# Optimization experiments

Measured on AMD Instinct MI355X. Metric: run time of the kernel, lower is better.

Reference implementation:

```python
import jax, jax.numpy as jnp
import numpy as np

B, N, F_, CI, C, CO = 2, 1024, 2048, 3, 80, 128
NB = 15          # DirResNet blocks
Q = C // 4


def _graph_bn(x, g, b, eps=1e-5):
    # BatchNorm over channels with stats over (batch, nodes) -- training-mode batch stats
    mu = jnp.mean(x, axis=(0, 1), keepdims=True)
    var = jnp.var(x, axis=(0, 1), keepdims=True)
    return (x - mu) * jax.lax.rsqrt(var + eps) * g + b


def _graph_conv(L, x, W0, W1, bias):
    # GraphConv with k=1: linear on [x, L @ x]
    return x @ W0 + jnp.einsum('bnm,bmc->bnc', L, x) @ W1 + bias


def _forward(inputs, L, Di, DiA, mask,
             conv1_W0, conv1_W1, conv1_b,
             rn_bn0_g, rn_bn0_b, rn_fc0_W, rn_fc0_b,
             rn_bn1_g, rn_bn1_b, rn_fc1_W, rn_fc1_b,
             bn1_g, bn1_b, bn2_g, bn2_b, bn3_g, bn3_b,
             conv2_W0, conv2_W1, conv2_b):
    v = _graph_conv(L, inputs, conv1_W0, conv1_W1, conv1_b)      # [B,N,C]
    f = jnp.zeros((B, F_, C), v.dtype)
    z = jnp.zeros_like(v)
    carry = (f, f, v, z, z)  # [f, tmp_f, v, tmp_v, tmp_v]

    def block(carry, p):
        f, tmp_f, v, tv0, tv1 = carry
        g0, b0, W0, c0, g1, b1, W1, c1 = p
        # Dirac: vertices -> faces (quaternion reshape: [B,N,C] -> [B,4N,C/4])
        Dv = jnp.matmul(Di, v.reshape(B, 4 * N, Q)).reshape(B, F_, C)
        x = jnp.concatenate([f, Dv], axis=-1)                    # [B,F,2C]
        f_new = jax.nn.elu(_graph_bn(x, g0, b0) @ W0 + c0) + tmp_f
        # Adjoint Dirac: faces -> vertices
        Df = jnp.matmul(DiA, f_new.reshape(B, 4 * F_, Q)).reshape(B, N, C)
        y = jnp.concatenate([v, Df], axis=-1)                    # [B,N,2C]
        v_new = jax.nn.elu(_graph_bn(y, g1, b1) @ W1 + c1) + tv0
        return (f_new, f, v_new, v, tv0), None

    carry, _ = jax.lax.scan(
        block, carry,
        (rn_bn0_g, rn_bn0_b, rn_fc0_W, rn_fc0_b,
         rn_bn1_g, rn_bn1_b, rn_fc1_W, rn_fc1_b))
    _, _, v2, v1, v0 = carry
    v = jax.nn.elu(_graph_bn(v2, bn1_g, bn1_b)
                   + _graph_bn(v1, bn2_g, bn2_b)
                   + _graph_bn(v0, bn3_g, bn3_b))
    # Dropout2d: identity (eval mode / deterministic reference)
    v = _graph_conv(L, v, conv2_W0, conv2_W1, conv2_b)           # [B,N,CO]
    out = (v * mask).sum(axis=1) / mask.sum(axis=1)              # masked mean pool -> [B,CO]
    return out


def setup_inputs() -> dict:
    key = jax.random.key(0)
    ks = jax.random.split(key, 32)
    s = 0.05
    d = {
        'inputs': jax.random.normal(ks[0], (B, N, CI), jnp.float32),
        'L': jax.random.normal(ks[1], (B, N, N), jnp.float32) / np.float32(np.sqrt(N)),
        'Di': jax.random.normal(ks[2], (B, 4 * F_, 4 * N), jnp.float32) / np.float32(np.sqrt(4 * N)),
        'DiA': jax.random.normal(ks[3], (B, 4 * N, 4 * F_), jnp.float32) / np.float32(np.sqrt(4 * F_)),
        'mask': (jax.random.uniform(ks[4], (B, N, 1)) > 0.2).astype(jnp.float32),
        'conv1_W0': jax.random.normal(ks[5], (CI, C), jnp.float32) * s,
        'conv1_W1': jax.random.normal(ks[6], (CI, C), jnp.float32) * s,
        'conv1_b': jax.random.normal(ks[7], (C,), jnp.float32) * s,
        'rn_bn0_g': 1.0 + 0.1 * jax.random.normal(ks[8], (NB, 2 * C), jnp.float32),
        'rn_bn0_b': s * jax.random.normal(ks[9], (NB, 2 * C), jnp.float32),
        'rn_fc0_W': jax.random.normal(ks[10], (NB, 2 * C, C), jnp.float32) * s,
        'rn_fc0_b': jax.random.normal(ks[11], (NB, C), jnp.float32) * s,
        'rn_bn1_g': 1.0 + 0.1 * jax.random.normal(ks[12], (NB, 2 * C), jnp.float32),
        'rn_bn1_b': s * jax.random.normal(ks[13], (NB, 2 * C), jnp.float32),
        'rn_fc1_W': jax.random.normal(ks[14], (NB, 2 * C, C), jnp.float32) * s,
        'rn_fc1_b': jax.random.normal(ks[15], (NB, C), jnp.float32) * s,
        'bn1_g': 1.0 + 0.1 * jax.random.normal(ks[16], (C,), jnp.float32),
        'bn1_b': s * jax.random.normal(ks[17], (C,), jnp.float32),
        'bn2_g': 1.0 + 0.1 * jax.random.normal(ks[18], (C,), jnp.float32),
        'bn2_b': s * jax.random.normal(ks[19], (C,), jnp.float32),
        'bn3_g': 1.0 + 0.1 * jax.random.normal(ks[20], (C,), jnp.float32),
        'bn3_b': s * jax.random.normal(ks[21], (C,), jnp.float32),
        'conv2_W0': jax.random.normal(ks[22], (C, CO), jnp.float32) * s,
        'conv2_W1': jax.random.normal(ks[23], (C, CO), jnp.float32) * s,
        'conv2_b': jax.random.normal(ks[24], (CO,), jnp.float32) * s,
    }
    return d


def reference(inputs, L, Di, DiA, mask,
              conv1_W0, conv1_W1, conv1_b,
              rn_bn0_g, rn_bn0_b, rn_fc0_W, rn_fc0_b,
              rn_bn1_g, rn_bn1_b, rn_fc1_W, rn_fc1_b,
              bn1_g, bn1_b, bn2_g, bn2_b, bn3_g, bn3_b,
              conv2_W0, conv2_W1, conv2_b):
    return _forward(inputs, L, Di, DiA, mask,
                    conv1_W0, conv1_W1, conv1_b,
                    rn_bn0_g, rn_bn0_b, rn_fc0_W, rn_fc0_b,
                    rn_bn1_g, rn_bn1_b, rn_fc1_W, rn_fc1_b,
                    bn1_g, bn1_b, bn2_g, bn2_b, bn3_g, bn3_b,
                    conv2_W0, conv2_W1, conv2_b)
```

## Files before the change

### kernel.cpp

```cpp
#include <hip/hip_runtime.h>
#include <cstdint>

#define BB 2
#define NN 1024
#define FF 2048
#define CC 80
#define C2 160
#define NB_ 15
#define ROWS_X (BB*FF)
#define ROWS_Y (BB*NN)
#define WTP 168

typedef __attribute__((ext_vector_type(8))) _Float16 half8;
typedef __attribute__((ext_vector_type(4))) _Float16 half4;
typedef __attribute__((ext_vector_type(4))) float f32x4;

__device__ __forceinline__ void softbar() {
  __builtin_amdgcn_sched_barrier(0);
  asm volatile("s_waitcnt lgkmcnt(0)" ::: "memory");
  __builtin_amdgcn_s_barrier();
  __builtin_amdgcn_sched_barrier(0);
}

__global__ __launch_bounds__(256) void k_conv1(
    const float* __restrict__ inp, const float* __restrict__ L,
    const float* __restrict__ W0, const float* __restrict__ W1,
    const float* __restrict__ bias, float* __restrict__ v,
    float4* __restrict__ vstat)
{
  int bx = blockIdx.x;
  int b = bx >> 6, rb = bx & 63;
  int row0 = rb * 16;
  __shared__ float red[256][3];
  __shared__ float lx[16][3];
  __shared__ float st[16][2][CC];
  int t = threadIdx.x;
  int rloc = t >> 4, sl = t & 15;
  const float* Lrow = L + ((size_t)b*NN + row0 + rloc) * NN;
  const float* ipb  = inp + (size_t)b*NN*3;
  float a0=0.f,a1=0.f,a2=0.f;
  for (int m = sl; m < NN; m += 16) {
    float lv = Lrow[m];
    a0 = fmaf(lv, ipb[m*3+0], a0);
    a1 = fmaf(lv, ipb[m*3+1], a1);
    a2 = fmaf(lv, ipb[m*3+2], a2);
  }
  red[t][0]=a0; red[t][1]=a1; red[t][2]=a2;
  __syncthreads();
  if (t < 48) {
    int row = t/3, ci = t%3;
    float s=0.f;
    for (int s2=0; s2<16; ++s2) s += red[row*16+s2][ci];
    lx[row][ci]=s;
  }
  __syncthreads();
  for (int o = t; o < 16*CC; o += 256) {
    int row = o/CC, c = o%CC;
    const float* ir = inp + ((size_t)b*NN + row0 + row)*3;
    float val = bias[c];
    #pragma unroll
    for (int ci=0; ci<3; ++ci)
      val += ir[ci]*W0[ci*CC+c] + lx[row][ci]*W1[ci*CC+c];
    v[((size_t)b*NN + row0 + row)*CC + c] = val;
    st[row][0][c] = val;
    st[row][1][c] = val*val;
  }
  __syncthreads();
  if (t < 40) {
    float s0=0.f,q0=0.f,s1=0.f,q1=0.f;
    for (int row=0; row<16; ++row){
      s0+=st[row][0][2*t];   q0+=st[row][1][2*t];
      s1+=st[row][0][2*t+1]; q1+=st[row][1][2*t+1];
    }
    vstat[(size_t)bx*40 + t] = make_float4(s0,q0,s1,q1);
  }
}

template<bool CVT>
__global__ __launch_bounds__(256) __attribute__((amdgpu_waves_per_eu(2,2)))
void k_dirac_mfma(
    const void* __restrict__ Ain, _Float16* __restrict__ Aout,
    const float* __restrict__ x,
    float* __restrict__ y, float4* __restrict__ stat, int M, int K)
{
  int b = blockIdx.y;
  x += (size_t)b*(size_t)K*20; y += (size_t)b*(size_t)M*20;
  const _Float16* Ah = (const _Float16*)Ain + (size_t)b*M*K;
  const float*    Af = (const float*)Ain    + (size_t)b*M*K;
  _Float16* Ao = CVT ? (Aout + (size_t)b*M*K) : nullptr;
  __shared__ _Float16 xT[2][2][32][264];
  __shared__ float cb_[2][8][64];
  __shared__ float stS[2][CC], stQ[2][CC];
  int t = threadIdx.x, lane = t & 63, w = t >> 6;
  int rw = w & 1, kh = w >> 1;
  int row0 = blockIdx.x*32 + rw*16;
  int cl = lane & 15, cg = lane >> 4;
  int KH = K >> 1;
  f32x4 acc0 = {0.f,0.f,0.f,0.f}, acc1 = {0.f,0.f,0.f,0.f};
  const float4* xv = (const float4*)x;
  int nchunk = KH >> 8;
  size_t aoff = (size_t)(row0 + cl)*K + (size_t)kh*KH + cg*8;

  for (int i = t; i < 2*2*12*264; i += 256) {
    int bb = i / (2*12*264);
    int rem = i - bb*(2*12*264);
    int hh = rem / (12*264);
    int r2 = rem - hh*(12*264);
    xT[bb][hh][20 + r2/264][r2 % 264] = (_Float16)0.f;
  }
  {
    float4 s0[5], s1[5];
    #pragma unroll
    for (int i=0;i<5;++i){ s0[i]=xv[(size_t)t*5+i]; s1[i]=xv[((size_t)KH+t)*5+i]; }
    #pragma unroll
    for (int i=0;i<5;++i){
      xT[0][0][4*i+0][t]=(_Float16)s0[i].x; xT[0][0][4*i+1][t]=(_Float16)s0[i].y;
      xT[0][0][4*i+2][t]=(_Float16)s0[i].z; xT[0][0][4*i+3][t]=(_Float16)s0[i].w;
      xT[0][1][4*i+0][t]=(_Float16)s1[i].x; xT[0][1][4*i+1][t]=(_Float16)s1[i].y;
      xT[0][1][4*i+2][t]=(_Float16)s1[i].z; xT[0][1][4*i+3][t]=(_Float16)s1[i].w;
    }
  }
  half8 a_cur[8];
  if constexpr (!CVT) {
    #pragma unroll
    for (int ks=0;ks<8;++ks) a_cur[ks] = *(const half8*)(Ah + aoff + ks*32);
  }
  __syncthreads();

  for (int c=0; c<nchunk; ++c) {
    int cur = c & 1;
    bool more = (c+1 < nchunk);
    float4 s0[5], s1[5];
    half8 a_nxt[8];
    if (more) {
      size_t k0 = (size_t)(c+1)*256 + t;
      #pragma unroll
      for (int i=0;i<5;++i){ s0[i]=xv[k0*5+i]; s1[i]=xv[(k0+KH)*5+i]; }
      if constexpr (!CVT) {
        const _Float16* An = Ah + aoff + (size_t)(c+1)*256;
        #pragma unroll
        for (int ks=0;ks<8;++ks) a_nxt[ks] = *(const half8*)(An + ks*32);
      }
    }
    if constexpr (CVT) {
      size_t ao = aoff + (size_t)c*256;
      #pragma unroll
      for (int ks=0;ks<8;++ks) {
        float4 f0 = *(const float4*)(Af + ao + ks*32);
        float4 f1 = *(const float4*)(Af + ao + ks*32 + 4);
        half8 a;
        a[0]=(_Float16)f0.x; a[1]=(_Float16)f0.y; a[2]=(_Float16)f0.z; a[3]=(_Float16)f0.w;
        a[4]=(_Float16)f1.x; a[5]=(_Float16)f1.y; a[6]=(_Float16)f1.z; a[7]=(_Float16)f1.w;
        a_cur[ks] = a;
        *(half8*)(Ao + ao + ks*32) = a;
      }
    }
    #pragma unroll
    for (int ks=0;ks<8;++ks) {
      half8 b0 = *(const half8*)(&xT[cur][kh][cl     ][ks*32 + cg*8]);
      half8 b1 = *(const half8*)(&xT[cur][kh][16 + cl][ks*32 + cg*8]);
      acc0 = __builtin_amdgcn_mfma_f32_16x16x32_f16(a_cur[ks], b0, acc0, 0,0,0);
      acc1 = __builtin_amdgcn_mfma_f32_16x16x32_f16(a_cur[ks], b1, acc1, 0,0,0);
    }
    if (more) {
      #pragma unroll
      for (int i=0;i<5;++i){
        xT[cur^1][0][4*i+0][t]=(_Float16)s0[i].x; xT[cur^1][0][4*i+1][t]=(_Float16)s0[i].y;
        xT[cur^1][0][4*i+2][t]=(_Float16)s0[i].z; xT[cur^1][0][4*i+3][t]=(_Float16)s0[i].w;
        xT[cur^1][1][4*i+0][t]=(_Float16)s1[i].x; xT[cur^1][1][4*i+1][t]=(_Float16)s1[i].y;
        xT[cur^1][1][4*i+2][t]=(_Float16)s1[i].z; xT[cur^1][1][4*i+3][t]=(_Float16)s1[i].w;
      }
      if constexpr (!CVT) {
        #pragma unroll
        for (int ks=0;ks<8;++ks) a_cur[ks] = a_nxt[ks];
      }
    }
    softbar();
  }

  if (kh == 1) {
    #pragma unroll
    for (int j=0;j<4;++j){ cb_[rw][j][lane]=acc0[j]; cb_[rw][4+j][lane]=acc1[j]; }
  }
  __syncthreads();
  if (kh == 0) {
    #pragma unroll
    for (int j=0;j<4;++j){ acc0[j]+=cb_[rw][j][lane]; acc1[j]+=cb_[rw][4+j][lane]; }
    #pragma unroll
    for (int j=0;j<4;++j) {
      float v = acc0[j];
      y[(size_t)(row0 + 4*cg + j)*20 + cl] = v;
      float s = v, sq = v*v;
      s  += __shfl_xor(s,16);  s  += __shfl_xor(s,32);
      sq += __shfl_xor(sq,16); sq += __shfl_xor(sq,32);
      if (cg==0) { stS[rw][j*20+cl]=s; stQ[rw][j*20+cl]=sq; }
    }
    #pragma unroll
    for (int j=0;j<4;++j) {
      float v = acc1[j];
      if (cl < 4) y[(size_t)(row0 + 4*cg + j)*20 + 16 + cl] = v;
      float s = v, sq = v*v;
      s  += __shfl_xor(s,16);  s  += __shfl_xor(s,32);
      sq += __shfl_xor(sq,16); sq += __shfl_xor(sq,32);
      if (cg==0 && cl<4) { stS[rw][j*20+16+cl]=s; stQ[rw][j*20+16+cl]=sq; }
    }
  }
  __syncthreads();
  int slot = blockIdx.y*gridDim.x + blockIdx.x;
  if (t < 40) {
    float4 o;
    o.x = stS[0][2*t]  +stS[1][2*t];
    o.y = stQ[0][2*t]  +stQ[1][2*t];
    o.z = stS[0][2*t+1]+stS[1][2*t+1];
    o.w = stQ[0][2*t+1]+stQ[1][2*t+1];
    stat[(size_t)slot*40 + t] = o;
  }
}

__global__ __launch_bounds__(256) __attribute__((amdgpu_waves_per_eu(2,2)))
void k_dirac_f32(
    const float* __restrict__ A, const float* __restrict__ x,
    float* __restrict__ y, float4* __restrict__ stat, int M, int K)
{
  const int DR = 4;
  int b = blockIdx.y;
  A += (size_t)b*M*K; x += (size_t)b*(size_t)K*20; y += (size_t)b*(size_t)M*20;
  __shared__ float xs[2][20][256];
  __shared__ float stS[4][CC], stQ[4][CC];
  int t = threadIdx.x, lane = t & 63, w = t >> 6;
  int row0 = blockIdx.x*(4*DR) + w*DR;
  float acc[DR][20];
  #pragma unroll
  for (int r=0;r<DR;++r)
    #pragma unroll
    for (int q=0;q<20;++q) acc[r][q]=0.f;
  const float4* xv = (const float4*)x;
  int nchunk = K >> 8;
  const float* Abase = A + (size_t)row0*K + (lane<<2);
  {
    float4 s0[5];
    #pragma unroll
    for (int i=0;i<5;++i) s0[i] = xv[(size_t)t*5 + i];
    #pragma unroll
    for (int i=0;i<5;++i) {
      xs[0][4*i+0][t]=s0[i].x; xs[0][4*i+1][t]=s0[i].y;
      xs[0][4*i+2][t]=s0[i].z; xs[0][4*i+3][t]=s0[i].w;
    }
  }
  float4 a[DR];
  #pragma unroll
  for (int r=0;r<DR;++r) a[r] = *(const float4*)(Abase + (size_t)r*K);
  __syncthreads();
  for (int c=0; c<nchunk; ++c) {
    int cur = c & 1;
    bool more = (c+1 < nchunk);
    float4 st[5];
    if (more) {
      size_t kb = (size_t)(c+1)*256 + t;
      #pragma unroll
      for (int i=0;i<5;++i) st[i] = xv[kb*5 + i];
    }
    float4 af[DR];
    #pragma unroll
    for (int r=0;r<DR;++r) af[r] = a[r];
    if (more) {
      const float* An = Abase + (size_t)(c+1)*256;
      #pragma unroll
      for (int r=0;r<DR;++r) a[r] = *(const float4*)(An + (size_t)r*K);
    }
    #pragma unroll
    for (int q=0;q<20;++q) {
      float4 xq = *(const float4*)(&xs[cur][q][lane<<2]);
      #pragma unroll
      for (int r=0;r<DR;++r) {
        acc[r][q] = fmaf(af[r].x, xq.x, acc[r][q]);
        acc[r][q] = fmaf(af[r].y, xq.y, acc[r][q]);
        acc[r][q] = fmaf(af[r].z, xq.z, acc[r][q]);
        acc[r][q] = fmaf(af[r].w, xq.w, acc[r][q]);
      }
    }
    if (more) {
      #pragma unroll
      for (int i=0;i<5;++i) {
        xs[cur^1][4*i+0][t]=st[i].x; xs[cur^1][4*i+1][t]=st[i].y;
        xs[cur^1][4*i+2][t]=st[i].z; xs[cur^1][4*i+3][t]=st[i].w;
      }
    }
    __syncthreads();
  }
  #pragma unroll
  for (int r=0;r<DR;++r) {
    #pragma unroll
    for (int q=0;q<20;++q) {
      float s = acc[r][q];
      s += __shfl_xor(s, 1);  s += __shfl_xor(s, 2);
      s += __shfl_xor(s, 4);  s += __shfl_xor(s, 8);
      s += __shfl_xor(s, 16); s += __shfl_xor(s, 32);
      acc[r][q]=s;
    }
    if (lane==0) {
      float4* yp = (float4*)(y + (size_t)(row0+r)*20);
      yp[0] = make_float4(acc[r][0],acc[r][1],acc[r][2],acc[r][3]);
      yp[1] = make_float4(acc[r][4],acc[r][5],acc[r][6],acc[r][7]);
      yp[2] = make_float4(acc[r][8],acc[r][9],acc[r][10],acc[r][11]);
      yp[3] = make_float4(acc[r][12],acc[r][13],acc[r][14],acc[r][15]);
      yp[4] = make_float4(acc[r][16],acc[r][17],acc[r][18],acc[r][19]);
    }
  }
  if (lane == 0) {
    #pragma unroll
    for (int r=0;r<DR;++r)
      #pragma unroll
      for (int q=0;q<20;++q) {
        float v0 = acc[r][q];
        stS[w][r*20+q] = v0;
        stQ[w][r*20+q] = v0*v0;
      }
  }
  __syncthreads();
  int slot = blockIdx.y*gridDim.x + blockIdx.x;
  if (t < 40) {
    float4 o;
    o.x = stS[0][2*t]+stS[1][2*t]+stS[2][2*t]+stS[3][2*t];
    o.y = stQ[0][2*t]+stQ[1][2*t]+stQ[2][2*t]+stQ[3][2*t];
    o.z = stS[0][2*t+1]+stS[1][2*t+1]+stS[2][2*t+1]+stS[3][2*t+1];
    o.w = stQ[0][2*t+1]+stQ[1][2*t+1]+stQ[2][2*t+1]+stQ[3][2*t+1];
    stat[(size_t)slot*40 + t] = o;
  }
}

__global__ __launch_bounds__(320) void k_fc(
    const float* __restrict__ p1, const float* __restrict__ p2,
    const float4* __restrict__ sp1, int ns1,
    const float4* __restrict__ sp2, int ns2,
    const float* __restrict__ g, const float* __restrict__ bb,
    const float* __restrict__ W, const float* __restrict__ cb,
    const float* add, float* out,
    float4* __restrict__ statout, int rows, float invrows)
{
  __shared__ _Float16 Wt[80*WTP];
  __shared__ _Float16 xh[16*WTP];
  __shared__ float ad[2][C2];
  __shared__ float bpl[CC];
  __shared__ float4 pst[2][2][40];
  __shared__ float stS[CC], stQ[CC];
  int t = threadIdx.x;
  int lane = t & 63, wv = t >> 6;
  int cl = lane & 15, cg = lane >> 4;
  int r0 = blockIdx.x * 16;

  if (t < 160) {
    int p = t % 40, s = (t/40) & 1, h = t/80;
    const float4* sp = s ? sp2 : sp1;
    int ns = s ? ns2 : ns1;
    int half = ns >> 1;
    const float4* base = sp + (size_t)(h*half)*40 + p;
    float4 acc = {0.f,0.f,0.f,0.f};
    int i=0;
    for (; i+8<=half; i+=8) {
      float4 v[8];
      #pragma unroll
      for (int j=0;j<8;++j) v[j] = base[(size_t)(i+j)*40];
      #pragma unroll
      for (int j=0;j<8;++j){ acc.x+=v[j].x; acc.y+=v[j].y; acc.z+=v[j].z; acc.w+=v[j].w; }
    }
    for (; i<half; ++i){
      float4 v = base[(size_t)i*40];
      acc.x+=v.x; acc.y+=v.y; acc.z+=v.z; acc.w+=v.w;
    }
    pst[h][s][p] = acc;
  } else {
    int t2 = t - 160;
    #pragma unroll
    for (int i=0;i<20;++i) {
      int f4 = t2 + i*160;
      float4 w4 = ((const float4*)W)[f4];
      int c2 = f4/20, c = (f4%20)*4;
      Wt[(c+0)*WTP + c2] = (_Float16)w4.x;
      Wt[(c+1)*WTP + c2] = (_Float16)w4.y;
      Wt[(c+2)*WTP + c2] = (_Float16)w4.z;
      Wt[(c+3)*WTP + c2] = (_Float16)w4.w;
    }
  }
  __syncthreads();

  half8 bfr[5];
  #pragma unroll
  for (int ks=0;ks<5;++ks)
    bfr[ks] = *(const half8*)(&Wt[(wv*16+cl)*WTP + ks*32 + cg*8]);
  if (t < C2) {
    int s = (t < CC) ? 0 : 1;
    int chl = (t < CC) ? t : t - CC;
    int p = chl >> 1, e = chl & 1;
    float4 a0 = pst[0][s][p], a1 = pst[1][s][p];
    float S = e ? (a0.z + a1.z) : (a0.x + a1.x);
    float Q = e ? (a0.w + a1.w) : (a0.y + a1.y);
    float mean = S*invrows;
    float var  = fmaf(-mean, mean, Q*invrows);
    float aa   = g[t]*rsqrtf(var + 1e-5f);
    ad[0][t]=aa; ad[1][t]= bb[t] - mean*aa;
  }
  __syncthreads();

  #pragma unroll
  for (int i=0;i<2;++i) {
    int f4 = t + i*320;
    if (f4 < 640) {
      int row = f4/40, cq = (f4%40)*4;
      const float* src = (cq < 80) ? (p1 + (size_t)(r0+row)*CC + cq)
                                   : (p2 + (size_t)(r0+row)*CC + cq - 80);
      float4 x4 = *(const float4*)src;
      half4 h4;
      h4[0]=(_Float16)(x4.x*ad[0][cq+0]); h4[1]=(_Float16)(x4.y*ad[0][cq+1]);
      h4[2]=(_Float16)(x4.z*ad[0][cq+2]); h4[3]=(_Float16)(x4.w*ad[0][cq+3]);
      *(half4*)(&xh[row*WTP + cq]) = h4;
    }
  }
  if (t < CC) {
    float s = cb[t];
    #pragma unroll
    for (int ks=0;ks<20;++ks) {
      half8 w8 = *(const half8*)(&Wt[t*WTP + ks*8]);
      #pragma unroll
      for (int j=0;j<8;++j) s = fmaf(ad[1][ks*8+j], (float)w8[j], s);
    }
    bpl[t]=s;
  }
  __syncthreads();

  half8 afr[5];
  #pragma unroll
  for (int ks=0;ks<5;++ks)
    afr[ks] = *(const half8*)(&xh[cl*WTP + ks*32 + cg*8]);
  f32x4 acc = {0.f,0.f,0.f,0.f};
  #pragma unroll
  for (int ks=0;ks<5;++ks)
    acc = __builtin_amdgcn_mfma_f32_16x16x32_f16(afr[ks], bfr[ks], acc, 0,0,0);
  float ss=0.f, sq=0.f;
  int col = wv*16 + cl;
  #pragma unroll
  for (int j=0;j<4;++j) {
    int row = r0 + 4*cg + j;
    float val = acc[j] + bpl[col];
    val = val>0.f ? val : expm1f(val);
    val += add[(size_t)row*CC + col];
    out[(size_t)row*CC + col] = val;
    ss += val; sq = fmaf(val,val,sq);
  }
  ss += __shfl_xor(ss,16); ss += __shfl_xor(ss,32);
  sq += __shfl_xor(sq,16); sq += __shfl_xor(sq,32);
  if (cg==0) { stS[col]=ss; stQ[col]=sq; }
  __syncthreads();
  if (t < 40)
    statout[(size_t)blockIdx.x*40 + t] = make_float4(stS[2*t], stQ[2*t], stS[2*t+1], stQ[2*t+1]);
}

__global__ __launch_bounds__(256) void k_final(
    const float* __restrict__ v2, const float* __restrict__ v1, const float* __restrict__ v0,
    const float4* __restrict__ s2, const float4* __restrict__ s1, const float4* __restrict__ s0,
    const float* __restrict__ g1, const float* __restrict__ b1,
    const float* __restrict__ g2, const float* __restrict__ b2,
    const float* __restrict__ g3, const float* __restrict__ b3,
    float* __restrict__ vf, int ns)
{
  __shared__ float A[3][CC], D[3][CC];
  __shared__ float4 pf[2][3][40];
  int t = threadIdx.x;
  if (t < 240) {
    int p = t % 40, s = (t/40) % 3, h = t/120;
    const float4* sp = s==0 ? s2 : (s==1 ? s1 : s0);
    int half = ns >> 1;
    const float4* base = sp + (size_t)(h*half)*40 + p;
    float4 acc = {0.f,0.f,0.f,0.f};
    int i=0;
    for (; i+8<=half; i+=8) {
      float4 v[8];
      #pragma unroll
      for (int j=0;j<8;++j) v[j] = base[(size_t)(i+j)*40];
      #pragma unroll
      for (int j=0;j<8;++j){ acc.x+=v[j].x; acc.y+=v[j].y; acc.z+=v[j].z; acc.w+=v[j].w; }
    }
    for (; i<half; ++i){
      float4 v = base[(size_t)i*40];
      acc.x+=v.x; acc.y+=v.y; acc.z+=v.z; acc.w+=v.w;
    }
    pf[h][s][p] = acc;
  }
  __syncthreads();
  if (t < 240) {
    int set = t/80, chl = t%80, p = chl>>1, e = chl&1;
    const float* gg  = set==0? g1 : (set==1? g2 : g3);
    const float* bbp = set==0? b1 : (set==1? b2 : b3);
    float4 a0 = pf[0][set][p], a1 = pf[1][set][p];
    float S = e ? (a0.z + a1.z) : (a0.x + a1.x);
    float Q = e ? (a0.w + a1.w) : (a0.y + a1.y);
    float mean = S*(1.f/ROWS_Y);
    float var  = fmaf(-mean,mean,Q*(1.f/ROWS_Y));
    float aa   = gg[chl]*rsqrtf(var+1e-5f);
    A[set][chl]=aa; D[set][chl]=bbp[chl]-mean*aa;
  }
  __syncthreads();
  for (size_t idx = (size_t)blockIdx.x*256 + t; idx < (size_t)ROWS_Y*CC; idx += (size_t)gridDim.x*256) {
    int c = (int)(idx % CC);
    float val = fmaf(v2[idx],A[0][c],D[0][c]) + fmaf(v1[idx],A[1][c],D[1][c]) + fmaf(v0[idx],A[2][c],D[2][c]);
    vf[idx] = val>0.f? val : expm1f(val);
  }
}

__global__ __launch_bounds__(256) void k_w(
    const float* __restrict__ mask, const float* __restrict__ L, float* __restrict__ w)
{
  int bx = blockIdx.x;
  int b = bx >> 4, n0 = (bx & 15) * 64;
  int t = threadIdx.x;
  int ks = t >> 6;
  __shared__ float red[4][64];
  float acc=0.f;
  const float* Lb = L + (size_t)b*NN*NN;
  const float* mb = mask + b*NN;
  int n = n0 + (t & 63);
  for (int k = ks*256; k < ks*256+256; k+=8) {
    float mv[8], lv[8];
    #pragma unroll
    for (int j=0;j<8;++j){ mv[j]=mb[k+j]; lv[j]=Lb[(size_t)(k+j)*NN + n]; }
    #pragma unroll
    for (int j=0;j<8;++j) acc = fmaf(mv[j], lv[j], acc);
  }
  red[ks][t&63]=acc;
  __syncthreads();
  if (t < 64) w[b*NN + n0 + t] = red[0][t]+red[1][t]+red[2][t]+red[3][t];
}

__global__ __launch_bounds__(256) void k_pool(
    const float* __restrict__ vf, const float* __restrict__ mask,
    const float* __restrict__ w, float* __restrict__ part)
{
  int bx = blockIdx.x;
  int b = bx >> 3, slab = bx & 7;
  int t = threadIdx.x, c = t%CC, rs = t/CC;
  __shared__ float st[3][2][CC];
  if (t<240) {
    float a1=0.f,a2=0.f;
    for (int r = rs; r < 128; r += 3) {
      int row = slab*128 + r;
      float val = vf[((size_t)b*NN + row)*CC + c];
      a1 = fmaf(mask[b*NN+row], val, a1);
      a2 = fmaf(w[b*NN+row],    val, a2);
    }
    st[rs][0][c]=a1; st[rs][1][c]=a2;
  }
  __syncthreads();
  if (t<CC) {
    part[((b*8+slab)*2+0)*CC+t] = st[0][0][t]+st[1][0][t]+st[2][0][t];
    part[((b*8+slab)*2+1)*CC+t] = st[0][1][t]+st[1][1][t]+st[2][1][t];
  }
}

__global__ __launch_bounds__(256) void k_out(
    const float* __restrict__ part, const float* __restrict__ mask,
    const float* __restrict__ W0, const float* __restrict__ W1,
    const float* __restrict__ b2, float* __restrict__ outp)
{
  __shared__ float pl[2][2][CC];
  __shared__ float msred[2][128];
  __shared__ float ms[2];
  int t = threadIdx.x;
  {
    int b = t >> 7, k0 = t & 127;
    float m[8];
    #pragma unroll
    for (int j=0;j<8;++j) m[j] = mask[b*NN + k0 + j*128];
    msred[b][k0] = ((m[0]+m[1])+(m[2]+m[3]))+((m[4]+m[5])+(m[6]+m[7]));
  }
  if (t < 160) {
    int b = t/CC, c = t%CC;
    float v1[8], v2[8];
    #pragma unroll
    for (int slab=0; slab<8; ++slab){
      v1[slab] = part[((b*8+slab)*2+0)*CC+c];
      v2[slab] = part[((b*8+slab)*2+1)*CC+c];
    }
    float s1=0.f,s2=0.f;
    #pragma unroll
    for (int slab=0;slab<8;++slab){ s1+=v1[slab]; s2+=v2[slab]; }
    pl[b][0][c]=s1; pl[b][1][c]=s2;
  }
  __syncthreads();
  if (t < 2) {
    float s=0.f;
    for (int k=0;k<128;++k) s += msred[t][k];
    ms[t]=s;
  }
  __syncthreads();
  int b = t >> 7, co = t & 127;
  float acc = 0.f;
  for (int c=0;c<CC;c+=8) {
    float w0[8], w1[8];
    #pragma unroll
    for (int j=0;j<8;++j){ w0[j]=W0[(c+j)*128+co]; w1[j]=W1[(c+j)*128+co]; }
    #pragma unroll
    for (int j=0;j<8;++j) acc += pl[b][0][c+j]*w0[j] + pl[b][1][c+j]*w1[j];
  }
  outp[t] = acc/ms[b] + b2[co];
}

extern "C" void kernel_launch(void* const* d_in, const int* in_sizes, int n_in,
                              void* d_out, int out_size, void* d_ws, size_t ws_size,
                              hipStream_t stream)
{
  const float* inp  = (const float*)d_in[0];
  const float* L    = (const float*)d_in[1];
  const float* Di   = (const float*)d_in[2];
  const float* DiA  = (const float*)d_in[3];
  const float* mask = (const float*)d_in[4];
  const float* c1W0 = (const float*)d_in[5];
  const float* c1W1 = (const float*)d_in[6];
  const float* c1b  = (const float*)d_in[7];
  const float* bn0g = (const float*)d_in[8];
  const float* bn0b = (const float*)d_in[9];
  const float* fc0W = (const float*)d_in[10];
  const float* fc0b = (const float*)d_in[11];
  const float* bn1g = (const float*)d_in[12];
  const float* bn1b = (const float*)d_in[13];
  const float* fc1W = (const float*)d_in[14];
  const float* fc1b = (const float*)d_in[15];
  const float* fbn1g= (const float*)d_in[16];
  const float* fbn1b= (const float*)d_in[17];
  const float* fbn2g= (const float*)d_in[18];
  const float* fbn2b= (const float*)d_in[19];
  const float* fbn3g= (const float*)d_in[20];
  const float* fbn3b= (const float*)d_in[21];
  const float* c2W0 = (const float*)d_in[22];
  const float* c2W1 = (const float*)d_in[23];
  const float* c2b  = (const float*)d_in[24];

  float* ws = (float*)d_ws;
  size_t off = 0;
  auto alloc = [&](size_t n)->float* { float* p = ws + off; off += (n + 63) & ~(size_t)63; return p; };
  const size_t STFL = (size_t)1024*40*4;
  float* vb[3];   for (int i=0;i<3;++i) vb[i]   = alloc((size_t)BB*NN*CC);
  float* fb[2];   for (int i=0;i<2;++i) fb[i]   = alloc((size_t)BB*FF*CC);
  float* Dv       = alloc((size_t)BB*FF*CC);
  float* Df       = alloc((size_t)BB*NN*CC);
  float4* vstat[3];for (int i=0;i<3;++i) vstat[i]= (float4*)alloc(STFL);
  float4* fstat[2];for (int i=0;i<2;++i) fstat[i]= (float4*)alloc(STFL);
  float4* dvstat  = (float4*)alloc(STFL);
  float4* dfstat  = (float4*)alloc(STFL);
  float* vf       = alloc((size_t)BB*NN*CC);
  float* wv       = alloc((size_t)BB*NN);
  float* part     = alloc((size_t)16*2*CC);
  const size_t nDi = (size_t)BB*(4*FF)*(4*NN);
  _Float16* Dih  = (_Float16*)alloc(nDi/2);
  _Float16* DiAh = (_Float16*)alloc(nDi/2);
  bool usebf = (off*sizeof(float) <= ws_size);

  hipMemsetAsync(fb[0],    0, (size_t)BB*FF*CC*4, stream);
  hipMemsetAsync(fb[1],    0, (size_t)BB*FF*CC*4, stream);
  hipMemsetAsync(vb[1],    0, (size_t)BB*NN*CC*4, stream);
  hipMemsetAsync(fstat[0], 0, (size_t)256*40*16, stream);

  k_conv1<<<128,256,0,stream>>>(inp, L, c1W0, c1W1, c1b, vb[0], vstat[0]);

  int nsDv = usebf ? 512 : 1024;
  int nsDf = usebf ? 256 : 512;
  int cur=0, p1=1, p2=2, fcur=0, fs=0;
  for (int it=0; it<NB_; ++it) {
    if (usebf) {
      if (it==0) k_dirac_mfma<true ><<<dim3(256,2),256,0,stream>>>(Di,  Dih, vb[cur], Dv, dvstat, 4*FF, 4*NN);
      else       k_dirac_mfma<false><<<dim3(256,2),256,0,stream>>>(Dih, Dih, vb[cur], Dv, dvstat, 4*FF, 4*NN);
    } else {
      k_dirac_f32<<<dim3(512,2),256,0,stream>>>(Di, vb[cur], Dv, dvstat, 4*FF, 4*NN);
    }
    k_fc<<<ROWS_X/16,320,0,stream>>>(fb[fcur], Dv, fstat[fs],256, dvstat,nsDv,
        bn0g+(size_t)it*C2, bn0b+(size_t)it*C2, fc0W+(size_t)it*C2*CC, fc0b+(size_t)it*CC,
        fb[1-fcur], fb[1-fcur], fstat[1-fs], ROWS_X, 1.f/ROWS_X);
    fcur = 1-fcur; fs = 1-fs;
    if (usebf) {
      if (it==0) k_dirac_mfma<true ><<<dim3(128,2),256,0,stream>>>(DiA,  DiAh, fb[fcur], Df, dfstat, 4*NN, 4*FF);
      else       k_dirac_mfma<false><<<dim3(128,2),256,0,stream>>>(DiAh, DiAh, fb[fcur], Df, dfstat, 4*NN, 4*FF);
    } else {
      k_dirac_f32<<<dim3(256,2),256,0,stream>>>(DiA, fb[fcur], Df, dfstat, 4*NN, 4*FF);
    }
    k_fc<<<ROWS_Y/16,320,0,stream>>>(vb[cur], Df, vstat[cur],128, dfstat,nsDf,
        bn1g+(size_t)it*C2, bn1b+(size_t)it*C2, fc1W+(size_t)it*C2*CC, fc1b+(size_t)it*CC,
        vb[p1], vb[p2], vstat[p2], ROWS_Y, 1.f/ROWS_Y);
    int tmp=p2; p2=p1; p1=cur; cur=tmp;
  }

  k_final<<<128,256,0,stream>>>(vb[cur],vb[p1],vb[p2], vstat[cur],vstat[p1],vstat[p2],
      fbn1g,fbn1b,fbn2g,fbn2b,fbn3g,fbn3b, vf, 128);
  k_w<<<32,256,0,stream>>>(mask, L, wv);
  k_pool<<<16,256,0,stream>>>(vf, mask, wv, part);
  k_out<<<1,256,0,stream>>>(part, mask, c2W0, c2W1, c2b, (float*)d_out);
}
```

Before: 1.922 ms.

## Emit pre-transposed fp16 activations from producers for the Dirac MFMA kernels

k_conv1 and k_fc now also write their outputs as an fp16, K-major transposed copy (xTv/xTf) laid out per quaternion channel. k_dirac_mfma then loads half8 vectors from this buffer straight into LDS, instead of reading fp32 rows and doing scalar convert-and-transpose stores. This cuts global read bytes and LDS store instructions in the Dirac kernels, at the cost of extra strided fp16 writes and a small LDS staging tile in k_fc. A stat reduction is also changed to zero out lanes that are not in use.

```diff
diff --git a/kernel.cpp b/kernel.cpp
--- a/kernel.cpp
+++ b/kernel.cpp
@@ -26,7 +26,7 @@
     const float* __restrict__ inp, const float* __restrict__ L,
     const float* __restrict__ W0, const float* __restrict__ W1,
     const float* __restrict__ bias, float* __restrict__ v,
-    float4* __restrict__ vstat)
+    float4* __restrict__ vstat, _Float16* __restrict__ vT)
 {
   int bx = blockIdx.x;
   int b = bx >> 6, rb = bx & 63;
@@ -62,6 +62,7 @@
     for (int ci=0; ci<3; ++ci)
       val += ir[ci]*W0[ci*CC+c] + lx[row][ci]*W1[ci*CC+c];
     v[((size_t)b*NN + row0 + row)*CC + c] = val;
+    vT[((size_t)b*32 + c%20)*(4*NN) + (row0+row)*4 + c/20] = (_Float16)val;
     st[row][0][c] = val;
     st[row][1][c] = val*val;
   }
@@ -80,14 +81,15 @@
 __global__ __launch_bounds__(256) __attribute__((amdgpu_waves_per_eu(2,2)))
 void k_dirac_mfma(
     const void* __restrict__ Ain, _Float16* __restrict__ Aout,
-    const float* __restrict__ x,
+    const _Float16* __restrict__ xTg,
     float* __restrict__ y, float4* __restrict__ stat, int M, int K)
 {
   int b = blockIdx.y;
-  x += (size_t)b*(size_t)K*20; y += (size_t)b*(size_t)M*20;
+  y += (size_t)b*(size_t)M*20;
   const _Float16* Ah = (const _Float16*)Ain + (size_t)b*M*K;
   const float*    Af = (const float*)Ain    + (size_t)b*M*K;
   _Float16* Ao = CVT ? (Aout + (size_t)b*M*K) : nullptr;
+  const _Float16* xTb = xTg + (size_t)b*32*K;
   __shared__ _Float16 xT[2][2][32][264];
   __shared__ float cb_[2][8][64];
   __shared__ float stS[2][CC], stQ[2][CC];
@@ -97,9 +99,16 @@
   int cl = lane & 15, cg = lane >> 4;
   int KH = K >> 1;
   f32x4 acc0 = {0.f,0.f,0.f,0.f}, acc1 = {0.f,0.f,0.f,0.f};
-  const float4* xv = (const float4*)x;
   int nchunk = KH >> 8;
   size_t aoff = (size_t)(row0 + cl)*K + (size_t)kh*KH + cg*8;
+  int i0 = t;
+  int h2_[5], q_[5], k8_[5];
+  #pragma unroll
+  for (int j=0;j<5;++j) {
+    int i = i0 + j*256;
+    h2_[j] = i/640; int rem = i - h2_[j]*640;
+    q_[j] = rem >> 5; k8_[j] = rem & 31;
+  }
 
   for (int i = t; i < 2*2*12*264; i += 256) {
     int bb = i / (2*12*264);
@@ -109,16 +118,13 @@
     xT[bb][hh][20 + r2/264][r2 % 264] = (_Float16)0.f;
   }
   {
-    float4 s0[5], s1[5];
-    #pragma unroll
-    for (int i=0;i<5;++i){ s0[i]=xv[(size_t)t*5+i]; s1[i]=xv[((size_t)KH+t)*5+i]; }
-    #pragma unroll
-    for (int i=0;i<5;++i){
-      xT[0][0][4*i+0][t]=(_Float16)s0[i].x; xT[0][0][4*i+1][t]=(_Float16)s0[i].y;
-      xT[0][0][4*i+2][t]=(_Float16)s0[i].z; xT[0][0][4*i+3][t]=(_Float16)s0[i].w;
-      xT[0][1][4*i+0][t]=(_Float16)s1[i].x; xT[0][1][4*i+1][t]=(_Float16)s1[i].y;
-      xT[0][1][4*i+2][t]=(_Float16)s1[i].z; xT[0][1][4*i+3][t]=(_Float16)s1[i].w;
-    }
+    half8 s[5];
+    #pragma unroll
+    for (int j=0;j<5;++j)
+      s[j] = *(const half8*)(xTb + (size_t)q_[j]*K + (size_t)h2_[j]*KH + k8_[j]*8);
+    #pragma unroll
+    for (int j=0;j<5;++j)
+      *(half8*)(&xT[0][h2_[j]][q_[j]][k8_[j]*8]) = s[j];
   }
   half8 a_cur[8];
   if constexpr (!CVT) {
@@ -130,12 +136,13 @@
   for (int c=0; c<nchunk; ++c) {
     int cur = c & 1;
     bool more = (c+1 < nchunk);
-    float4 s0[5], s1[5];
+    half8 s[5];
     half8 a_nxt[8];
     if (more) {
-      size_t k0 = (size_t)(c+1)*256 + t;
-      #pragma unroll
-      for (int i=0;i<5;++i){ s0[i]=xv[k0*5+i]; s1[i]=xv[(k0+KH)*5+i]; }
+      #pragma unroll
+      for (int j=0;j<5;++j)
+        s[j] = *(const half8*)(xTb + (size_t)q_[j]*K + (size_t)h2_[j]*KH
+                               + (size_t)(c+1)*256 + k8_[j]*8);
       if constexpr (!CVT) {
         const _Float16* An = Ah + aoff + (size_t)(c+1)*256;
         #pragma unroll
@@ -164,12 +171,8 @@
     }
     if (more) {
       #pragma unroll
-      for (int i=0;i<5;++i){
-        xT[cur^1][0][4*i+0][t]=(_Float16)s0[i].x; xT[cur^1][0][4*i+1][t]=(_Float16)s0[i].y;
-        xT[cur^1][0][4*i+2][t]=(_Float16)s0[i].z; xT[cur^1][0][4*i+3][t]=(_Float16)s0[i].w;
-        xT[cur^1][1][4*i+0][t]=(_Float16)s1[i].x; xT[cur^1][1][4*i+1][t]=(_Float16)s1[i].y;
-        xT[cur^1][1][4*i+2][t]=(_Float16)s1[i].z; xT[cur^1][1][4*i+3][t]=(_Float16)s1[i].w;
-      }
+      for (int j=0;j<5;++j)
+        *(half8*)(&xT[cur^1][h2_[j]][q_[j]][k8_[j]*8]) = s[j];
       if constexpr (!CVT) {
         #pragma unroll
         for (int ks=0;ks<8;++ks) a_cur[ks] = a_nxt[ks];
@@ -199,7 +202,7 @@
     for (int j=0;j<4;++j) {
       float v = acc1[j];
       if (cl < 4) y[(size_t)(row0 + 4*cg + j)*20 + 16 + cl] = v;
-      float s = v, sq = v*v;
+      float s = (cl<4)? v : 0.f, sq = (cl<4)? v*v : 0.f;
       s  += __shfl_xor(s,16);  s  += __shfl_xor(s,32);
       sq += __shfl_xor(sq,16); sq += __shfl_xor(sq,32);
       if (cg==0 && cl<4) { stS[rw][j*20+16+cl]=s; stQ[rw][j*20+16+cl]=sq; }
@@ -336,10 +339,12 @@
     const float* __restrict__ g, const float* __restrict__ bb,
     const float* __restrict__ W, const float* __restrict__ cb,
     const float* add, float* out,
-    float4* __restrict__ statout, int rows, float invrows)
+    float4* __restrict__ statout, int rows, float invrows,
+    _Float16* __restrict__ xTout, int rpbs)
 {
   __shared__ _Float16 Wt[80*WTP];
   __shared__ _Float16 xh[16*WTP];
+  __shared__ _Float16 xtt[20][68];
   __shared__ float ad[2][C2];
   __shared__ float bpl[CC];
   __shared__ float4 pst[2][2][40];
@@ -438,6 +443,7 @@
     acc = __builtin_amdgcn_mfma_f32_16x16x32_f16(afr[ks], bfr[ks], acc, 0,0,0);
   float ss=0.f, sq=0.f;
   int col = wv*16 + cl;
+  int q20 = col % 20, c4 = col / 20;
   #pragma unroll
   for (int j=0;j<4;++j) {
     int row = r0 + 4*cg + j;
@@ -445,12 +451,21 @@
     val = val>0.f ? val : expm1f(val);
     val += add[(size_t)row*CC + col];
     out[(size_t)row*CC + col] = val;
+    xtt[q20][(4*cg+j)*4 + c4] = (_Float16)val;
     ss += val; sq = fmaf(val,val,sq);
   }
   ss += __shfl_xor(ss,16); ss += __shfl_xor(ss,32);
   sq += __shfl_xor(sq,16); sq += __shfl_xor(sq,32);
   if (cg==0) { stS[col]=ss; stQ[col]=sq; }
   __syncthreads();
+  if (t < 160) {
+    int q = t/8, k8 = t%8;
+    size_t Kx = (size_t)4 << rpbs;
+    int bb2 = r0 >> rpbs;
+    int rl  = r0 & ((1<<rpbs)-1);
+    half8 v = *(const half8*)(&xtt[q][k8*8]);
+    *(half8*)(xTout + ((size_t)bb2*32 + q)*Kx + (size_t)rl*4 + k8*8) = v;
+  }
   if (t < 40)
     statout[(size_t)blockIdx.x*40 + t] = make_float4(stS[2*t], stQ[2*t], stS[2*t+1], stQ[2*t+1]);
 }
@@ -649,6 +664,8 @@
   float* vf       = alloc((size_t)BB*NN*CC);
   float* wv       = alloc((size_t)BB*NN);
   float* part     = alloc((size_t)16*2*CC);
+  _Float16* xTv   = (_Float16*)alloc((size_t)BB*32*(4*NN)/2);
+  _Float16* xTf   = (_Float16*)alloc((size_t)BB*32*(4*FF)/2);
   const size_t nDi = (size_t)BB*(4*FF)*(4*NN);
   _Float16* Dih  = (_Float16*)alloc(nDi/2);
   _Float16* DiAh = (_Float16*)alloc(nDi/2);
@@ -659,31 +676,31 @@
   hipMemsetAsync(vb[1],    0, (size_t)BB*NN*CC*4, stream);
   hipMemsetAsync(fstat[0], 0, (size_t)256*40*16, stream);
 
-  k_conv1<<<128,256,0,stream>>>(inp, L, c1W0, c1W1, c1b, vb[0], vstat[0]);
+  k_conv1<<<128,256,0,stream>>>(inp, L, c1W0, c1W1, c1b, vb[0], vstat[0], xTv);
 
   int nsDv = usebf ? 512 : 1024;
   int nsDf = usebf ? 256 : 512;
   int cur=0, p1=1, p2=2, fcur=0, fs=0;
   for (int it=0; it<NB_; ++it) {
     if (usebf) {
-      if (it==0) k_dirac_mfma<true ><<<dim3(256,2),256,0,stream>>>(Di,  Dih, vb[cur], Dv, dvstat, 4*FF, 4*NN);
-      else       k_dirac_mfma<false><<<dim3(256,2),256,0,stream>>>(Dih, Dih, vb[cur], Dv, dvstat, 4*FF, 4*NN);
+      if (it==0) k_dirac_mfma<true ><<<dim3(256,2),256,0,stream>>>(Di,  Dih, xTv, Dv, dvstat, 4*FF, 4*NN);
+      else       k_dirac_mfma<false><<<dim3(256,2),256,0,stream>>>(Dih, Dih, xTv, Dv, dvstat, 4*FF, 4*NN);
     } else {
       k_dirac_f32<<<dim3(512,2),256,0,stream>>>(Di, vb[cur], Dv, dvstat, 4*FF, 4*NN);
     }
     k_fc<<<ROWS_X/16,320,0,stream>>>(fb[fcur], Dv, fstat[fs],256, dvstat,nsDv,
         bn0g+(size_t)it*C2, bn0b+(size_t)it*C2, fc0W+(size_t)it*C2*CC, fc0b+(size_t)it*CC,
-        fb[1-fcur], fb[1-fcur], fstat[1-fs], ROWS_X, 1.f/ROWS_X);
+        fb[1-fcur], fb[1-fcur], fstat[1-fs], ROWS_X, 1.f/ROWS_X, xTf, 11);
     fcur = 1-fcur; fs = 1-fs;
     if (usebf) {
-      if (it==0) k_dirac_mfma<true ><<<dim3(128,2),256,0,stream>>>(DiA,  DiAh, fb[fcur], Df, dfstat, 4*NN, 4*FF);
-      else       k_dirac_mfma<false><<<dim3(128,2),256,0,stream>>>(DiAh, DiAh, fb[fcur], Df, dfstat, 4*NN, 4*FF);
+      if (it==0) k_dirac_mfma<true ><<<dim3(128,2),256,0,stream>>>(DiA,  DiAh, xTf, Df, dfstat, 4*NN, 4*FF);
+      else       k_dirac_mfma<false><<<dim3(128,2),256,0,stream>>>(DiAh, DiAh, xTf, Df, dfstat, 4*NN, 4*FF);
     } else {
       k_dirac_f32<<<dim3(256,2),256,0,stream>>>(DiA, fb[fcur], Df, dfstat, 4*NN, 4*FF);
     }
     k_fc<<<ROWS_Y/16,320,0,stream>>>(vb[cur], Df, vstat[cur],128, dfstat,nsDf,
         bn1g+(size_t)it*C2, bn1b+(size_t)it*C2, fc1W+(size_t)it*C2*CC, fc1b+(size_t)it*CC,
-        vb[p1], vb[p2], vstat[p2], ROWS_Y, 1.f/ROWS_Y);
+        vb[p1], vb[p2], vstat[p2], ROWS_Y, 1.f/ROWS_Y, xTv, 10);
     int tmp=p2; p2=p1; p1=cur; cur=tmp;
   }
 
```

Measured after the change: 1.729 ms. 1.11x faster.
